# Performance work log

Measured on AMD Instinct MI355X. Metric: run time of the kernel, lower is better.

## Reference

```python
import jax, jax.numpy as jnp
import numpy as np

N = 600000          # points
V = 120000          # occupied voxels (60k per sample)
BEV_H = 512
BEV_W = 512
B = 2
BN_EPS = 1e-3


def setup_inputs() -> dict:
    key = jax.random.key(0)
    k1, k2, k3, k4, k5 = jax.random.split(key, 5)
    bev_coordinate = jax.random.normal(k1, (N, 3), jnp.float32) * 20.0
    bev_local_coordinate = jax.random.normal(k2, (N, 3), jnp.float32)
    intensity = jax.random.uniform(k3, (N,), jnp.float32)
    bev_mapping_pv = jax.random.randint(k4, (N,), 0, V, jnp.int32)
    # unique (batch, h, w) per voxel: 60k voxels/sample spread over 512*512 grid
    v = np.arange(V)
    per_batch = V // B
    flat = (v % per_batch) * (BEV_H * BEV_W // per_batch)  # stride 4, unique
    bev_mapping_vf = jnp.asarray(
        np.stack([v // per_batch, flat // BEV_W, flat % BEV_W], axis=1),
        dtype=jnp.int32)
    W = jax.random.normal(k5, (64, 10), jnp.float32) * (1.0 / np.sqrt(10))
    gamma = jnp.ones((64,), jnp.float32)
    beta = jnp.zeros((64,), jnp.float32)
    return {
        "bev_coordinate": bev_coordinate,
        "bev_local_coordinate": bev_local_coordinate,
        "intensity": intensity,
        "bev_mapping_pv": bev_mapping_pv,
        "bev_mapping_vf": bev_mapping_vf,
        "W": W,
        "gamma": gamma,
        "beta": beta,
        "batch_size": B,
    }


def reference(bev_coordinate, bev_local_coordinate, intensity,
              bev_mapping_pv, bev_mapping_vf, W, gamma, beta, batch_size):
    nvox = bev_mapping_vf.shape[0]
    pv = bev_mapping_pv
    # scatterMean: per-voxel mean of coordinates, gathered back per point
    counts = jnp.zeros((nvox,), bev_coordinate.dtype).at[pv].add(1.0)
    sums = jnp.zeros((nvox, 3), bev_coordinate.dtype).at[pv].add(bev_coordinate)
    vox_mean = sums / jnp.maximum(counts, 1.0)[:, None]
    point_mean = vox_mean[pv]                              # [N,3]
    # feature: [coord(3), intensity(1), coord-mean(3), local(3)] -> [N,10]
    feature = jnp.concatenate(
        [bev_coordinate, intensity[:, None],
         bev_coordinate - point_mean, bev_local_coordinate], axis=1)
    # Linear(10,64,bias=False) + BatchNorm1d(train mode, batch stats) + ReLU
    x = feature @ W.T                                      # [N,64]
    mu = jnp.mean(x, axis=0)
    var = jnp.mean(jnp.square(x - mu), axis=0)             # biased, as torch BN
    x = (x - mu) * jax.lax.rsqrt(var + BN_EPS) * gamma + beta
    x = jax.nn.relu(x)
    # scatterMax into voxels, empty voxels stay at finfo.min (as torch impl)
    vox_max = jnp.full((nvox, 64), jnp.finfo(x.dtype).min, x.dtype).at[pv].max(x)
    # dense scatter_nd into [B,H,W,64], then channels_first
    dense = jnp.zeros((batch_size, BEV_H, BEV_W, 64), x.dtype)
    dense = dense.at[bev_mapping_vf[:, 0], bev_mapping_vf[:, 1],
                     bev_mapping_vf[:, 2]].set(vox_max)
    return jnp.transpose(dense, (0, 3, 1, 2))              # [B,64,H,W]
```

## Files before the change

kernel.cpp:

```cpp
#include <hip/hip_runtime.h>
#include <float.h>

#define EMPTY_FILL (-3.3895313892515355e38f)

#define HW 262144
#define BEVW 512
#define NBPM 256



__global__ void k_init(int* counts, int V, int* inv, int ncell) {
    int i = blockIdx.x * blockDim.x + threadIdx.x;
    int st = gridDim.x * blockDim.x;
    for (int t = i; t < V; t += st) counts[t] = 0;
    for (int t = i; t < ncell; t += st) inv[t] = -1;
}

__global__ void k_count(const int* __restrict__ pv, int n, int* __restrict__ counts) {
    int i = blockIdx.x * blockDim.x + threadIdx.x;
    if (i < n) atomicAdd(&counts[pv[i]], 1);
}

__global__ void k_scan1(const int* __restrict__ counts, int V, int* __restrict__ partials) {
    __shared__ int sh[256];
    int base = blockIdx.x * 2048;
    int s = 0;
    for (int e = 0; e < 8; ++e) {
        int idx = base + e * 256 + threadIdx.x;
        if (idx < V) s += counts[idx];
    }
    sh[threadIdx.x] = s; __syncthreads();
    for (int d = 128; d > 0; d >>= 1) {
        if (threadIdx.x < d) sh[threadIdx.x] += sh[threadIdx.x + d];
        __syncthreads();
    }
    if (threadIdx.x == 0) partials[blockIdx.x] = sh[0];
}

__global__ void k_scan2(const int* __restrict__ partials, int NB, int* __restrict__ blockoff) {
    __shared__ int sh[256];
    int run = 0;
    for (int base = 0; base < NB; base += 256) {
        int idx = base + threadIdx.x;
        int p = (idx < NB) ? partials[idx] : 0;
        __syncthreads();
        sh[threadIdx.x] = p; __syncthreads();
        for (int d = 1; d < 256; d <<= 1) {
            int v2 = sh[threadIdx.x];
            if (threadIdx.x >= d) v2 += sh[threadIdx.x - d];
            __syncthreads(); sh[threadIdx.x] = v2; __syncthreads();
        }
        if (idx < NB) blockoff[idx] = run + sh[threadIdx.x] - p;
        run += sh[255];
    }
}

__global__ void k_scan3(const int* __restrict__ counts, int V,
                        const int* __restrict__ blockoff, int* __restrict__ cursor) {
    __shared__ int sh[256];
    int t = threadIdx.x;
    int base = blockIdx.x * 2048 + t * 8;
    int c[8]; int s = 0;
#pragma unroll
    for (int e = 0; e < 8; ++e) {
        int idx = base + e;
        c[e] = (idx < V) ? counts[idx] : 0;
        s += c[e];
    }
    sh[t] = s; __syncthreads();
    for (int d = 1; d < 256; d <<= 1) {
        int v2 = sh[t];
        if (t >= d) v2 += sh[t - d];
        __syncthreads(); sh[t] = v2; __syncthreads();
    }
    int run = blockoff[blockIdx.x] + sh[t] - s;
#pragma unroll
    for (int e = 0; e < 8; ++e) {
        int idx = base + e;
        if (idx < V) cursor[idx] = run;
        run += c[e];
    }
}

__global__ void k_fill(const int* __restrict__ pv,
                       const float* __restrict__ coord,
                       const float* __restrict__ locc,
                       const float* __restrict__ inten, int n,
                       int* __restrict__ cursor,
                       float4* __restrict__ pdata) {
    int i = blockIdx.x * blockDim.x + threadIdx.x;
    if (i >= n) return;
    int pos = atomicAdd(&cursor[pv[i]], 1);
    pdata[2*pos]   = make_float4(coord[3*i], coord[3*i+1], coord[3*i+2], inten[i]);
    pdata[2*pos+1] = make_float4(locc[3*i],  locc[3*i+1],  locc[3*i+2],  0.f);
}

__global__ void k_pmoments(const float* __restrict__ coord,
                           const float* __restrict__ locc,
                           const float* __restrict__ inten, int n,
                           float* __restrict__ parts) {
    __shared__ float sm[35];
    if (threadIdx.x < 35) sm[threadIdx.x] = 0.f;
    __syncthreads();
    float acc[35];
#pragma unroll
    for (int t = 0; t < 35; ++t) acc[t] = 0.f;
    int i = blockIdx.x * blockDim.x + threadIdx.x;
    int st = gridDim.x * blockDim.x;
    for (; i < n; i += st) {
        float r[7];
        r[0] = coord[3*i]; r[1] = coord[3*i+1]; r[2] = coord[3*i+2];
        r[3] = inten[i];
        r[4] = locc[3*i]; r[5] = locc[3*i+1]; r[6] = locc[3*i+2];
        int t = 0;
#pragma unroll
        for (int j = 0; j < 7; ++j)
#pragma unroll
            for (int k = j; k < 7; ++k) { acc[t] += r[j]*r[k]; ++t; }
#pragma unroll
        for (int j = 0; j < 7; ++j) acc[28+j] += r[j];
    }
#pragma unroll
    for (int t = 0; t < 35; ++t) {
        float x = acc[t];
#pragma unroll
        for (int m = 1; m < 64; m <<= 1) x += __shfl_xor(x, m, 64);
        acc[t] = x;
    }
    if ((threadIdx.x & 63) == 0) {
#pragma unroll
        for (int t = 0; t < 35; ++t) atomicAdd(&sm[t], acc[t]);
    }
    __syncthreads();
    if (threadIdx.x < 35) parts[blockIdx.x * 35 + threadIdx.x] = sm[threadIdx.x];
}

__global__ void k_voxstat(const float4* __restrict__ pdata,
                          const int* __restrict__ counts,
                          const int* __restrict__ cursor, int V,
                          float* __restrict__ vmean,
                          float* __restrict__ parts) {
    __shared__ float sm[18];
    if (threadIdx.x < 18) sm[threadIdx.x] = 0.f;
    __syncthreads();
    int v = blockIdx.x * blockDim.x + threadIdx.x;
    float acc[18];
#pragma unroll
    for (int t = 0; t < 18; ++t) acc[t] = 0.f;
    if (v < V) {
        int cnt = counts[v];
        int end = cursor[v];
        int st = end - cnt;
        float s0=0.f,s1=0.f,s2=0.f,si=0.f,l0=0.f,l1=0.f,l2=0.f;
        for (int k = st; k < end; ++k) {
            float4 a = pdata[2*k];
            float4 b = pdata[2*k+1];
            s0 += a.x; s1 += a.y; s2 += a.z; si += a.w;
            l0 += b.x; l1 += b.y; l2 += b.z;
        }
        float inv_ = 1.f / fmaxf((float)cnt, 1.f);
        float m0 = s0*inv_, m1 = s1*inv_, m2 = s2*inv_;
        vmean[3*v] = m0; vmean[3*v+1] = m1; vmean[3*v+2] = m2;
        float cf = (float)cnt;
        acc[0]=cf*m0*m0; acc[1]=cf*m0*m1; acc[2]=cf*m0*m2;
        acc[3]=cf*m1*m1; acc[4]=cf*m1*m2; acc[5]=cf*m2*m2;
        acc[6]=m0*si; acc[7]=m1*si; acc[8]=m2*si;
        acc[9]=m0*l0;  acc[10]=m0*l1; acc[11]=m0*l2;
        acc[12]=m1*l0; acc[13]=m1*l1; acc[14]=m1*l2;
        acc[15]=m2*l0; acc[16]=m2*l1; acc[17]=m2*l2;
    }
#pragma unroll
    for (int t = 0; t < 18; ++t) {
        float x = acc[t];
#pragma unroll
        for (int m = 1; m < 64; m <<= 1) x += __shfl_xor(x, m, 64);
        acc[t] = x;
    }
    if ((threadIdx.x & 63) == 0) {
#pragma unroll
        for (int t = 0; t < 18; ++t) atomicAdd(&sm[t], acc[t]);
    }
    __syncthreads();
    if (threadIdx.x < 18) parts[blockIdx.x * 18 + threadIdx.x] = sm[threadIdx.x];
}

__global__ void k_bn_final(const float* __restrict__ pm, int nbpm,
                           const float* __restrict__ pvs, int nbvs,
                           const float* __restrict__ W,
                           const float* __restrict__ gamma,
                           const float* __restrict__ beta,
                           int n, float* __restrict__ ss) {
    __shared__ double red[53][16];
    __shared__ double g[53];
    __shared__ double MF[10][10];
    __shared__ double SF[10];
    int tid = threadIdx.x;
    int t16 = tid >> 4;
    int l16 = tid & 15;
    double s = 0.0;
    if (t16 < 35) {
        for (int b = l16; b < nbpm; b += 16) s += (double)pm[b * 35 + t16];
        red[t16][l16] = s;
    } else if (t16 < 53) {
        int u = t16 - 35;
        for (int b = l16; b < nbvs; b += 16) s += (double)pvs[b * 18 + u];
        red[t16][l16] = s;
    }
    __syncthreads();
    if (tid < 53) {
        double a = 0.0;
#pragma unroll
        for (int k = 0; k < 16; ++k) a += red[tid][k];
        g[tid] = a;
    }
    __syncthreads();
    if (tid == 0) {
        double M7[7][7], S7[7], Pmm[3][3], Qmi[3], Rml[3][3];
        int t = 0;
        for (int j = 0; j < 7; ++j)
            for (int k = j; k < 7; ++k) { M7[j][k] = M7[k][j] = g[t]; ++t; }
        for (int j = 0; j < 7; ++j) S7[j] = g[28+j];
        t = 35;
        for (int j = 0; j < 3; ++j)
            for (int k = j; k < 3; ++k) { Pmm[j][k] = Pmm[k][j] = g[t]; ++t; }
        for (int k = 0; k < 3; ++k) Qmi[k] = g[41+k];
        for (int j = 0; j < 3; ++j)
            for (int k = 0; k < 3; ++k) Rml[j][k] = g[44+3*j+k];
        const int rmap[10] = {0,1,2,3,-1,-1,-1,4,5,6};
        for (int a = 0; a < 10; ++a)
            for (int b = a; b < 10; ++b) {
                bool ad = (a >= 4 && a < 7), bd = (b >= 4 && b < 7);
                double val;
                if (!ad && !bd) val = M7[rmap[a]][rmap[b]];
                else if (ad && bd) val = M7[a-4][b-4] - Pmm[a-4][b-4];
                else {
                    int k = ad ? a-4 : b-4;
                    int o = ad ? b : a;
                    int ro = rmap[o];
                    double X;
                    if (o < 3) X = Pmm[o][k];
                    else if (o == 3) X = Qmi[k];
                    else X = Rml[k][ro-4];
                    val = M7[ro][k] - X;
                }
                MF[a][b] = MF[b][a] = val;
            }
        for (int a = 0; a < 10; ++a)
            SF[a] = (a >= 4 && a < 7) ? 0.0 : S7[rmap[a]];
    }
    __syncthreads();
    int c = tid;
    if (c >= 64) return;
    double w[10];
    for (int j = 0; j < 10; ++j) w[j] = (double)W[c*10+j];
    double invn = 1.0 / (double)n;
    double mu = 0.0;
    for (int j = 0; j < 10; ++j) mu += w[j] * SF[j] * invn;
    double ex2 = 0.0;
    for (int j = 0; j < 10; ++j) {
        double sj = 0.0;
        for (int k = 0; k < 10; ++k) sj += MF[j][k] * w[k];
        ex2 += w[j] * sj;
    }
    ex2 *= invn;
    double var = ex2 - mu*mu;
    double scale = (double)gamma[c] / sqrt(var + 1e-3);
    double shift = (double)beta[c] - mu*scale;
    ss[c] = (float)scale;
    ss[64+c] = (float)shift;
}

__global__ void k_vox(const float4* __restrict__ pdata,
                      const int* __restrict__ counts,
                      const int* __restrict__ cursor,
                      const float* __restrict__ vmean,
                      const int* __restrict__ vf, int V,
                      const float* __restrict__ W,
                      const float* __restrict__ ss,
                      float* __restrict__ vfeat,
                      int* __restrict__ inv) {
    const int lane = threadIdx.x & 63;
    const int v = blockIdx.x * (blockDim.x >> 6) + (threadIdx.x >> 6);
    if (v >= V) return;
    float wr[10];
#pragma unroll
    for (int j = 0; j < 10; ++j) wr[j] = W[lane*10 + j];
    const float scale = ss[lane];
    const float shift = ss[64 + lane];
    const float su0 = (wr[0]+wr[4])*scale, su1 = (wr[1]+wr[5])*scale,
                su2 = (wr[2]+wr[6])*scale, sw3 = wr[3]*scale,
                sw7 = wr[7]*scale, sw8 = wr[8]*scale, sw9 = wr[9]*scale;
    const int cnt = counts[v];
    float m;
    if (cnt == 0) {
        m = EMPTY_FILL;
    } else {
        const int end = cursor[v];
        const int st = end - cnt;
        const float off = shift - (wr[4]*vmean[3*v] + wr[5]*vmean[3*v+1]
                                   + wr[6]*vmean[3*v+2]) * scale;
        m = -FLT_MAX;
        for (int k = st; k < end; ++k) {
            float4 a = pdata[2*k];
            float4 b = pdata[2*k+1];
            float y = su0*a.x + su1*a.y + su2*a.z + sw3*a.w
                    + sw7*b.x + sw8*b.y + sw9*b.z + off;
            m = fmaxf(m, y);
        }
        m = fmaxf(m, 0.f);
    }
    vfeat[(size_t)v*64 + lane] = m;
    if (lane == 0) {
        int b = vf[3*v], h = vf[3*v+1], w = vf[3*v+2];
        inv[b*HW + h*BEVW + w] = v;
    }
}

__global__ void k_out(const float* __restrict__ vfeat,
                      const int* __restrict__ inv,
                      int ncell, float* __restrict__ out) {
    int cell = blockIdx.x * blockDim.x + threadIdx.x;
    if (cell >= ncell) return;
    int v = inv[cell];
    int b = cell >> 18;
    int hw = cell & (HW - 1);
    float* ob = out + ((size_t)b << 24) + hw;
    const float4* vb = (const float4*)(vfeat + (size_t)(v >= 0 ? v : 0) * 64);
#pragma unroll
    for (int c0 = 0; c0 < 16; ++c0) {
        float4 q = (v >= 0) ? vb[c0] : make_float4(0.f, 0.f, 0.f, 0.f);
        ob[(size_t)(4*c0+0) * HW] = q.x;
        ob[(size_t)(4*c0+1) * HW] = q.y;
        ob[(size_t)(4*c0+2) * HW] = q.z;
        ob[(size_t)(4*c0+3) * HW] = q.w;
    }
}


__global__ void k_zero4(float4* a, long na, float4* b, long nb) {
    long i = (long)blockIdx.x * blockDim.x + threadIdx.x;
    long st = (long)gridDim.x * blockDim.x;
    float4 z = make_float4(0.f, 0.f, 0.f, 0.f);
    for (long t = i; t < na; t += st) a[t] = z;
    for (long t = i; t < nb; t += st) b[t] = z;
}

__global__ void k_scatter_mean7(const float* __restrict__ coord,
                                const float* __restrict__ locc,
                                const float* __restrict__ inten,
                                const int* __restrict__ pv, int n,
                                float* __restrict__ countsf,
                                float* __restrict__ sums7) {
    int i = blockIdx.x * blockDim.x + threadIdx.x;
    if (i >= n) return;
    int v = pv[i];
    atomicAdd(&countsf[v], 1.0f);
    atomicAdd(&sums7[7*v+0], coord[3*i+0]);
    atomicAdd(&sums7[7*v+1], coord[3*i+1]);
    atomicAdd(&sums7[7*v+2], coord[3*i+2]);
    atomicAdd(&sums7[7*v+3], inten[i]);
    atomicAdd(&sums7[7*v+4], locc[3*i+0]);
    atomicAdd(&sums7[7*v+5], locc[3*i+1]);
    atomicAdd(&sums7[7*v+6], locc[3*i+2]);
}

__global__ void k_vstat_fb(const float* __restrict__ countsf,
                           const float* __restrict__ sums7, int V,
                           float* __restrict__ vmean, float* __restrict__ parts) {
    __shared__ float sm[18];
    if (threadIdx.x < 18) sm[threadIdx.x] = 0.f;
    __syncthreads();
    int v = blockIdx.x * blockDim.x + threadIdx.x;
    float acc[18];
#pragma unroll
    for (int t = 0; t < 18; ++t) acc[t] = 0.f;
    if (v < V) {
        float cf = countsf[v];
        float inv_ = 1.f / fmaxf(cf, 1.f);
        float m0 = sums7[7*v]*inv_, m1 = sums7[7*v+1]*inv_, m2 = sums7[7*v+2]*inv_;
        float si = sums7[7*v+3], l0 = sums7[7*v+4], l1 = sums7[7*v+5], l2 = sums7[7*v+6];
        vmean[3*v] = m0; vmean[3*v+1] = m1; vmean[3*v+2] = m2;
        acc[0]=cf*m0*m0; acc[1]=cf*m0*m1; acc[2]=cf*m0*m2;
        acc[3]=cf*m1*m1; acc[4]=cf*m1*m2; acc[5]=cf*m2*m2;
        acc[6]=m0*si; acc[7]=m1*si; acc[8]=m2*si;
        acc[9]=m0*l0;  acc[10]=m0*l1; acc[11]=m0*l2;
        acc[12]=m1*l0; acc[13]=m1*l1; acc[14]=m1*l2;
        acc[15]=m2*l0; acc[16]=m2*l1; acc[17]=m2*l2;
    }
#pragma unroll
    for (int t = 0; t < 18; ++t) {
        float x = acc[t];
#pragma unroll
        for (int m = 1; m < 64; m <<= 1) x += __shfl_xor(x, m, 64);
        acc[t] = x;
    }
    if ((threadIdx.x & 63) == 0) {
#pragma unroll
        for (int t = 0; t < 18; ++t) atomicAdd(&sm[t], acc[t]);
    }
    __syncthreads();
    if (threadIdx.x < 18) parts[blockIdx.x * 18 + threadIdx.x] = sm[threadIdx.x];
}

__global__ void k_scatter_max_dense(const float* __restrict__ coord,
                                    const float* __restrict__ locc,
                                    const float* __restrict__ inten,
                                    const int* __restrict__ pv, int n,
                                    const float* __restrict__ vmean,
                                    const float* __restrict__ W,
                                    const float* __restrict__ ss,
                                    const int* __restrict__ vf,
                                    unsigned int* __restrict__ outbits) {
    const int lane = threadIdx.x & 63;
    const int wave = blockIdx.x * (blockDim.x >> 6) + (threadIdx.x >> 6);
    const int nwaves = gridDim.x * (blockDim.x >> 6);
    float wr[10];
#pragma unroll
    for (int j = 0; j < 10; ++j) wr[j] = W[lane*10 + j];
    const float scale = ss[lane];
    const float shift = ss[64 + lane];
    const int cpw = (n + nwaves - 1) / nwaves;
    const int p0 = wave * cpw;
    const int p1 = (p0 + cpw < n) ? (p0 + cpw) : n;
    for (int p = p0; p < p1; ++p) {
        int v = pv[p];
        float c0 = coord[3*p], c1 = coord[3*p+1], c2 = coord[3*p+2];
        float x = wr[0]*c0 + wr[1]*c1 + wr[2]*c2 + wr[3]*inten[p]
                + wr[4]*(c0-vmean[3*v]) + wr[5]*(c1-vmean[3*v+1]) + wr[6]*(c2-vmean[3*v+2])
                + wr[7]*locc[3*p] + wr[8]*locc[3*p+1] + wr[9]*locc[3*p+2];
        float y = fmaxf(x*scale + shift, 0.0f);
        int b = vf[3*v], h = vf[3*v+1], w = vf[3*v+2];
        size_t idx = (((size_t)b*64 + lane)*BEVW + h)*BEVW + w;
        atomicMax(&outbits[idx], __float_as_uint(y));
    }
}

__global__ void k_fix_empty_dense(const float* __restrict__ countsf,
                                  const int* __restrict__ vf, int V,
                                  float* __restrict__ out) {
    int v = blockIdx.x * blockDim.x + threadIdx.x;
    if (v >= V) return;
    if (countsf[v] > 0.f) return;
    int b = vf[3*v], h = vf[3*v+1], w = vf[3*v+2];
    for (int c = 0; c < 64; ++c)
        out[(((size_t)b*64 + c)*BEVW + h)*BEVW + w] = EMPTY_FILL;
}


static inline size_t rup(size_t x) { return (x + 255) & ~(size_t)255; }

extern "C" void kernel_launch(void* const* d_in, const int* in_sizes, int n_in,
                              void* d_out, int out_size, void* d_ws, size_t ws_size,
                              hipStream_t stream) {
    const float* coord = (const float*)d_in[0];
    const float* locc  = (const float*)d_in[1];
    const float* inten = (const float*)d_in[2];
    const int*   pv    = (const int*)d_in[3];
    const int*   vf    = (const int*)d_in[4];
    const float* W     = (const float*)d_in[5];
    const float* gamma = (const float*)d_in[6];
    const float* beta  = (const float*)d_in[7];
    const int n = in_sizes[2];
    const int V = in_sizes[4] / 3;
    const int B = out_size / (64 * HW);
    const int ncell = B * HW;
    const int NB = (V + 2047) / 2048;
    const int vxblk = (V + 255) / 256;
    const int ptblk = (n + 255) / 256;

    char* ws = (char*)d_ws;
    size_t off = 0;
    int*   counts   = (int*)(ws + off);   off = rup(off + (size_t)V * 4);
    int*   cursor   = (int*)(ws + off);   off = rup(off + (size_t)V * 4);
    int*   partials = (int*)(ws + off);   off = rup(off + (size_t)NB * 4);
    int*   blockoff = (int*)(ws + off);   off = rup(off + (size_t)NB * 4);
    float* parts_pm = (float*)(ws + off); off = rup(off + (size_t)NBPM * 35 * 4);
    float* parts_vs = (float*)(ws + off); off = rup(off + (size_t)vxblk * 18 * 4);
    float* ss       = (float*)(ws + off); off = rup(off + 512);
    float* vmean    = (float*)(ws + off); off = rup(off + (size_t)V * 12);
    int*   inv      = (int*)(ws + off);   off = rup(off + (size_t)ncell * 4);
    float* vfeat    = (float*)(ws + off); off = rup(off + (size_t)V * 256);
    bool big = (ws_size >= off) && ((size_t)out_size * 4 >= (size_t)n * 32);

    float4* pdata = (float4*)d_out;

    if (big) {
        k_init<<<2048, 256, 0, stream>>>(counts, V, inv, ncell);
        k_count<<<ptblk, 256, 0, stream>>>(pv, n, counts);
        k_scan1<<<NB, 256, 0, stream>>>(counts, V, partials);
        k_scan2<<<1, 256, 0, stream>>>(partials, NB, blockoff);
        k_scan3<<<NB, 256, 0, stream>>>(counts, V, blockoff, cursor);
        k_fill<<<ptblk, 256, 0, stream>>>(pv, coord, locc, inten, n, cursor, pdata);
        k_pmoments<<<NBPM, 256, 0, stream>>>(coord, locc, inten, n, parts_pm);
        k_voxstat<<<vxblk, 256, 0, stream>>>(pdata, counts, cursor, V, vmean, parts_vs);
        k_bn_final<<<1, 1024, 0, stream>>>(parts_pm, NBPM, parts_vs, vxblk,
                                           W, gamma, beta, n, ss);
        k_vox<<<(V + 3) / 4, 256, 0, stream>>>(pdata, counts, cursor, vmean,
                                               vf, V, W, ss, vfeat, inv);
        k_out<<<(ncell + 255) / 256, 256, 0, stream>>>(vfeat, inv, ncell, (float*)d_out);
    } else {
        size_t o2 = 0;
        float* countsf  = (float*)(ws + o2); o2 = rup(o2 + (size_t)V * 4);
        float* sums7    = (float*)(ws + o2); o2 = rup(o2 + (size_t)V * 28);
        float* parts_p2 = (float*)(ws + o2); o2 = rup(o2 + (size_t)NBPM * 35 * 4);
        float* parts_v2 = (float*)(ws + o2); o2 = rup(o2 + (size_t)vxblk * 18 * 4);
        float* ss2      = (float*)(ws + o2); o2 = rup(o2 + 512);
        float* vmean2   = (float*)(ws + o2); o2 = rup(o2 + (size_t)V * 12);
        k_zero4<<<2048, 256, 0, stream>>>((float4*)ws, (long)(o2 / 16),
                                          (float4*)d_out, (long)out_size / 4);
        k_scatter_mean7<<<ptblk, 256, 0, stream>>>(coord, locc, inten, pv, n,
                                                   countsf, sums7);
        k_pmoments<<<NBPM, 256, 0, stream>>>(coord, locc, inten, n, parts_p2);
        k_vstat_fb<<<vxblk, 256, 0, stream>>>(countsf, sums7, V, vmean2, parts_v2);
        k_bn_final<<<1, 1024, 0, stream>>>(parts_p2, NBPM, parts_v2, vxblk,
                                           W, gamma, beta, n, ss2);
        k_scatter_max_dense<<<2048, 256, 0, stream>>>(coord, locc, inten, pv, n,
                                                      vmean2, W, ss2, vf,
                                                      (unsigned int*)d_out);
        k_fix_empty_dense<<<vxblk, 256, 0, stream>>>(countsf, vf, V, (float*)d_out);
    }
}
```

Baseline: 215.3 us.

## Accumulate voxel sums with atomics in fill; persistent waves in voxel max kernel

The fill kernel now atomically accumulates the per-voxel sums of coordinates, intensity and local coordinates. The voxel-stat kernel reads those sums directly instead of re-reading the sorted point buffer, which removes one full pass over the points. The voxel max kernel switches to a fixed grid of 2048 blocks, with each wave handling a contiguous range of voxels, and the per-voxel offset is added once after the max instead of per point. The cost is 4.2M extra float atomics in the fill kernel and a non-deterministic summation order.

Measured after the change: 404.2 us. 87.8% more time.

```diff
diff --git a/kernel.cpp b/kernel.cpp
--- a/kernel.cpp
+++ b/kernel.cpp
@@ -9,11 +9,13 @@
 
 
 
-__global__ void k_init(int* counts, int V, int* inv, int ncell) {
+__global__ void k_init(int* counts, int V, int* inv, int ncell, float* sums7) {
     int i = blockIdx.x * blockDim.x + threadIdx.x;
     int st = gridDim.x * blockDim.x;
     for (int t = i; t < V; t += st) counts[t] = 0;
     for (int t = i; t < ncell; t += st) inv[t] = -1;
+    int n7 = 7 * V;
+    for (int t = i; t < n7; t += st) sums7[t] = 0.f;
 }
 
 __global__ void k_count(const int* __restrict__ pv, int n, int* __restrict__ counts) {
@@ -87,12 +89,24 @@
                        const float* __restrict__ locc,
                        const float* __restrict__ inten, int n,
                        int* __restrict__ cursor,
-                       float4* __restrict__ pdata) {
+                       float4* __restrict__ pdata,
+                       float* __restrict__ sums7) {
     int i = blockIdx.x * blockDim.x + threadIdx.x;
     if (i >= n) return;
-    int pos = atomicAdd(&cursor[pv[i]], 1);
-    pdata[2*pos]   = make_float4(coord[3*i], coord[3*i+1], coord[3*i+2], inten[i]);
-    pdata[2*pos+1] = make_float4(locc[3*i],  locc[3*i+1],  locc[3*i+2],  0.f);
+    int v = pv[i];
+    float c0 = coord[3*i], c1 = coord[3*i+1], c2 = coord[3*i+2];
+    float it = inten[i];
+    float l0 = locc[3*i], l1 = locc[3*i+1], l2 = locc[3*i+2];
+    int pos = atomicAdd(&cursor[v], 1);
+    pdata[2*pos]   = make_float4(c0, c1, c2, it);
+    pdata[2*pos+1] = make_float4(l0, l1, l2, 0.f);
+    atomicAdd(&sums7[7*v+0], c0);
+    atomicAdd(&sums7[7*v+1], c1);
+    atomicAdd(&sums7[7*v+2], c2);
+    atomicAdd(&sums7[7*v+3], it);
+    atomicAdd(&sums7[7*v+4], l0);
+    atomicAdd(&sums7[7*v+5], l1);
+    atomicAdd(&sums7[7*v+6], l2);
 }
 
 __global__ void k_pmoments(const float* __restrict__ coord,
@@ -135,11 +149,9 @@
     if (threadIdx.x < 35) parts[blockIdx.x * 35 + threadIdx.x] = sm[threadIdx.x];
 }
 
-__global__ void k_voxstat(const float4* __restrict__ pdata,
-                          const int* __restrict__ counts,
-                          const int* __restrict__ cursor, int V,
-                          float* __restrict__ vmean,
-                          float* __restrict__ parts) {
+__global__ void k_vstat(const int* __restrict__ counts,
+                        const float* __restrict__ sums7, int V,
+                        float* __restrict__ vmean, float* __restrict__ parts) {
     __shared__ float sm[18];
     if (threadIdx.x < 18) sm[threadIdx.x] = 0.f;
     __syncthreads();
@@ -148,20 +160,11 @@
 #pragma unroll
     for (int t = 0; t < 18; ++t) acc[t] = 0.f;
     if (v < V) {
-        int cnt = counts[v];
-        int end = cursor[v];
-        int st = end - cnt;
-        float s0=0.f,s1=0.f,s2=0.f,si=0.f,l0=0.f,l1=0.f,l2=0.f;
-        for (int k = st; k < end; ++k) {
-            float4 a = pdata[2*k];
-            float4 b = pdata[2*k+1];
-            s0 += a.x; s1 += a.y; s2 += a.z; si += a.w;
-            l0 += b.x; l1 += b.y; l2 += b.z;
-        }
-        float inv_ = 1.f / fmaxf((float)cnt, 1.f);
-        float m0 = s0*inv_, m1 = s1*inv_, m2 = s2*inv_;
+        float cf = (float)counts[v];
+        float inv_ = 1.f / fmaxf(cf, 1.f);
+        float m0 = sums7[7*v]*inv_, m1 = sums7[7*v+1]*inv_, m2 = sums7[7*v+2]*inv_;
+        float si = sums7[7*v+3], l0 = sums7[7*v+4], l1 = sums7[7*v+5], l2 = sums7[7*v+6];
         vmean[3*v] = m0; vmean[3*v+1] = m1; vmean[3*v+2] = m2;
-        float cf = (float)cnt;
         acc[0]=cf*m0*m0; acc[1]=cf*m0*m1; acc[2]=cf*m0*m2;
         acc[3]=cf*m1*m1; acc[4]=cf*m1*m2; acc[5]=cf*m2*m2;
         acc[6]=m0*si; acc[7]=m1*si; acc[8]=m2*si;
@@ -280,8 +283,12 @@
                       float* __restrict__ vfeat,
                       int* __restrict__ inv) {
     const int lane = threadIdx.x & 63;
-    const int v = blockIdx.x * (blockDim.x >> 6) + (threadIdx.x >> 6);
-    if (v >= V) return;
+    const int wave = blockIdx.x * (blockDim.x >> 6) + (threadIdx.x >> 6);
+    const int nw = gridDim.x * (blockDim.x >> 6);
+    const int vpw = (V + nw - 1) / nw;
+    const int v0 = wave * vpw;
+    if (v0 >= V) return;
+    const int v1 = (v0 + vpw < V) ? (v0 + vpw) : V;
     float wr[10];
 #pragma unroll
     for (int j = 0; j < 10; ++j) wr[j] = W[lane*10 + j];
@@ -289,30 +296,32 @@
     const float shift = ss[64 + lane];
     const float su0 = (wr[0]+wr[4])*scale, su1 = (wr[1]+wr[5])*scale,
                 su2 = (wr[2]+wr[6])*scale, sw3 = wr[3]*scale,
-                sw7 = wr[7]*scale, sw8 = wr[8]*scale, sw9 = wr[9]*scale;
-    const int cnt = counts[v];
-    float m;
-    if (cnt == 0) {
-        m = EMPTY_FILL;
-    } else {
+                sw7 = wr[7]*scale, sw8 = wr[8]*scale, sw9 = wr[9]*scale,
+                sv0 = wr[4]*scale, sv1 = wr[5]*scale, sv2 = wr[6]*scale;
+    for (int v = v0; v < v1; ++v) {
+        const int cnt = counts[v];
         const int end = cursor[v];
-        const int st = end - cnt;
-        const float off = shift - (wr[4]*vmean[3*v] + wr[5]*vmean[3*v+1]
-                                   + wr[6]*vmean[3*v+2]) * scale;
-        m = -FLT_MAX;
-        for (int k = st; k < end; ++k) {
-            float4 a = pdata[2*k];
-            float4 b = pdata[2*k+1];
-            float y = su0*a.x + su1*a.y + su2*a.z + sw3*a.w
-                    + sw7*b.x + sw8*b.y + sw9*b.z + off;
-            m = fmaxf(m, y);
+        float m;
+        if (cnt == 0) {
+            m = EMPTY_FILL;
+        } else {
+            const float off = shift - (sv0*vmean[3*v] + sv1*vmean[3*v+1]
+                                       + sv2*vmean[3*v+2]);
+            float mm = -FLT_MAX;
+#pragma unroll 2
+            for (int k = end - cnt; k < end; ++k) {
+                float4 a = pdata[2*k];
+                float4 b = pdata[2*k+1];
+                float y = su0*a.x + su1*a.y + su2*a.z + sw3*a.w
+                        + sw7*b.x + sw8*b.y + sw9*b.z;
+                mm = fmaxf(mm, y);
+            }
+            m = fmaxf(mm + off, 0.f);
         }
-        m = fmaxf(m, 0.f);
-    }
-    vfeat[(size_t)v*64 + lane] = m;
-    if (lane == 0) {
-        int b = vf[3*v], h = vf[3*v+1], w = vf[3*v+2];
-        inv[b*HW + h*BEVW + w] = v;
+        vfeat[(size_t)v*64 + lane] = m;
+        if (lane == 0) {
+            inv[vf[3*v]*HW + vf[3*v+1]*BEVW + vf[3*v+2]] = v;
+        }
     }
 }
 
@@ -478,6 +487,7 @@
     float* parts_vs = (float*)(ws + off); off = rup(off + (size_t)vxblk * 18 * 4);
     float* ss       = (float*)(ws + off); off = rup(off + 512);
     float* vmean    = (float*)(ws + off); off = rup(off + (size_t)V * 12);
+    float* sums7    = (float*)(ws + off); off = rup(off + (size_t)V * 28);
     int*   inv      = (int*)(ws + off);   off = rup(off + (size_t)ncell * 4);
     float* vfeat    = (float*)(ws + off); off = rup(off + (size_t)V * 256);
     bool big = (ws_size >= off) && ((size_t)out_size * 4 >= (size_t)n * 32);
@@ -485,23 +495,24 @@
     float4* pdata = (float4*)d_out;
 
     if (big) {
-        k_init<<<2048, 256, 0, stream>>>(counts, V, inv, ncell);
+        k_init<<<2048, 256, 0, stream>>>(counts, V, inv, ncell, sums7);
         k_count<<<ptblk, 256, 0, stream>>>(pv, n, counts);
         k_scan1<<<NB, 256, 0, stream>>>(counts, V, partials);
         k_scan2<<<1, 256, 0, stream>>>(partials, NB, blockoff);
         k_scan3<<<NB, 256, 0, stream>>>(counts, V, blockoff, cursor);
-        k_fill<<<ptblk, 256, 0, stream>>>(pv, coord, locc, inten, n, cursor, pdata);
+        k_fill<<<ptblk, 256, 0, stream>>>(pv, coord, locc, inten, n, cursor,
+                                          pdata, sums7);
         k_pmoments<<<NBPM, 256, 0, stream>>>(coord, locc, inten, n, parts_pm);
-        k_voxstat<<<vxblk, 256, 0, stream>>>(pdata, counts, cursor, V, vmean, parts_vs);
+        k_vstat<<<vxblk, 256, 0, stream>>>(counts, sums7, V, vmean, parts_vs);
         k_bn_final<<<1, 1024, 0, stream>>>(parts_pm, NBPM, parts_vs, vxblk,
                                            W, gamma, beta, n, ss);
-        k_vox<<<(V + 3) / 4, 256, 0, stream>>>(pdata, counts, cursor, vmean,
-                                               vf, V, W, ss, vfeat, inv);
+        k_vox<<<2048, 256, 0, stream>>>(pdata, counts, cursor, vmean,
+                                        vf, V, W, ss, vfeat, inv);
         k_out<<<(ncell + 255) / 256, 256, 0, stream>>>(vfeat, inv, ncell, (float*)d_out);
     } else {
         size_t o2 = 0;
         float* countsf  = (float*)(ws + o2); o2 = rup(o2 + (size_t)V * 4);
-        float* sums7    = (float*)(ws + o2); o2 = rup(o2 + (size_t)V * 28);
+        float* sums7b   = (float*)(ws + o2); o2 = rup(o2 + (size_t)V * 28);
         float* parts_p2 = (float*)(ws + o2); o2 = rup(o2 + (size_t)NBPM * 35 * 4);
         float* parts_v2 = (float*)(ws + o2); o2 = rup(o2 + (size_t)vxblk * 18 * 4);
         float* ss2      = (float*)(ws + o2); o2 = rup(o2 + 512);
@@ -509,9 +520,9 @@
         k_zero4<<<2048, 256, 0, stream>>>((float4*)ws, (long)(o2 / 16),
                                           (float4*)d_out, (long)out_size / 4);
         k_scatter_mean7<<<ptblk, 256, 0, stream>>>(coord, locc, inten, pv, n,
-                                                   countsf, sums7);
+                                                   countsf, sums7b);
         k_pmoments<<<NBPM, 256, 0, stream>>>(coord, locc, inten, n, parts_p2);
-        k_vstat_fb<<<vxblk, 256, 0, stream>>>(countsf, sums7, V, vmean2, parts_v2);
+        k_vstat_fb<<<vxblk, 256, 0, stream>>>(countsf, sums7b, V, vmean2, parts_v2);
         k_bn_final<<<1, 1024, 0, stream>>>(parts_p2, NBPM, parts_v2, vxblk,
                                            W, gamma, beta, n, ss2);
         k_scatter_max_dense<<<2048, 256, 0, stream>>>(coord, locc, inten, pv, n,
```
